# Kernel optimization log

Hardware: AMD Instinct MI355X
Metric: run time of the kernel (lower is better)

The kernel has to match this reference:

```python
import jax, jax.numpy as jnp
import numpy as np

N, HID, MAXD, B, NCLS, GRUH = 50000, 128, 16, 50, 10, 32


def setup_inputs() -> dict:
    key = jax.random.key(0)
    ks = jax.random.split(key, 18)
    s = 0.05
    nrm = lambda k, shp: (jax.random.normal(k, shp, jnp.float32) * s)
    return {
        "feature": jax.random.normal(ks[0], (N, HID), jnp.float32),
        "nbr_idx": jax.random.randint(ks[1], (N, MAXD), 0, N, dtype=jnp.int32),
        "deg": jax.random.randint(ks[2], (N,), 1, MAXD + 1, dtype=jnp.int32),
        "graph_ids": (jnp.arange(N, dtype=jnp.int32) * B) // N,
        # SAGEConv(lstm) params: LSTM(in=HID, hidden=HID) + fc_self/fc_neigh
        "lstm_Wih": nrm(ks[3], (4 * HID, HID)),
        "lstm_Whh": nrm(ks[4], (4 * HID, HID)),
        "lstm_bih": nrm(ks[5], (4 * HID,)),
        "lstm_bhh": nrm(ks[6], (4 * HID,)),
        "W_self": nrm(ks[7], (HID, HID)),
        "W_neigh": nrm(ks[8], (HID, HID)),
        "b_sage": nrm(ks[9], (HID,)),
        # GraphConv params
        "W_gc": nrm(ks[10], (HID, HID)),
        "b_gc": nrm(ks[11], (HID,)),
        # GRU params (h0=0 so weight_hh contributes nothing; only its bias matters)
        "Wih_gru": nrm(ks[12], (3 * GRUH, HID)),
        "bih_gru": nrm(ks[13], (3 * GRUH,)),
        "bhh_gru": nrm(ks[14], (3 * GRUH,)),
        # classifier (dropout is identity at eval)
        "W_cls": nrm(ks[15], (GRUH, NCLS)),
        "b_cls": nrm(ks[16], (NCLS,)),
    }


def _lstm_aggregate(feats, nbr_idx, deg, Wih, Whh, bih, bhh):
    # DGL SAGEConv 'lstm' reducer: run LSTM over each node's neighbor features,
    # take final hidden state. Implemented as a masked scan over padded lists.
    n, hdim = feats.shape
    h0 = jnp.zeros((n, hdim), feats.dtype)

    def step(carry, t):
        h, c = carry
        x = feats[jnp.take(nbr_idx, t, axis=1)]  # [N, HID] gather of t-th neighbor
        gates = x @ Wih.T + bih + h @ Whh.T + bhh
        i, f, g, o = jnp.split(gates, 4, axis=-1)  # torch gate order i,f,g,o
        c_new = jax.nn.sigmoid(f) * c + jax.nn.sigmoid(i) * jnp.tanh(g)
        h_new = jax.nn.sigmoid(o) * jnp.tanh(c_new)
        valid = (t < deg)[:, None]
        return (jnp.where(valid, h_new, h), jnp.where(valid, c_new, c)), None

    (hT, _), _ = jax.lax.scan(step, (h0, h0), jnp.arange(nbr_idx.shape[1]))
    return hT  # hidden at each node's last valid neighbor


def _graph_conv(h, nbr_idx, deg, W, b):
    # DGL GraphConv norm='both': D^-1/2 A D^-1/2 h W + b
    n, maxd = nbr_idx.shape
    norm = jax.lax.rsqrt(jnp.maximum(deg.astype(h.dtype), 1.0))
    hn = h * norm[:, None]
    mask = (jnp.arange(maxd, dtype=jnp.int32)[None, :] < deg[:, None]).astype(h.dtype)
    contrib = hn[nbr_idx.reshape(-1)] * mask.reshape(-1)[:, None]  # [N*MAXD, HID]
    dst = jnp.repeat(jnp.arange(n, dtype=jnp.int32), maxd)
    agg = jax.ops.segment_sum(contrib, dst, num_segments=n)
    return (agg * norm[:, None]) @ W + b


def _gru_step(x, Wih, bih, bhh):
    # single GRU step with h0 = 0 (seq_len == 1 in the original view(1, N, H))
    gh = x @ Wih.T + bih  # [N, 3*GRUH]
    xr, xz, xn = jnp.split(gh, 3, axis=-1)  # torch gate order r,z,n
    br, bz, bn = jnp.split(bhh, 3)
    r = jax.nn.sigmoid(xr + br)
    z = jax.nn.sigmoid(xz + bz)
    nst = jnp.tanh(xn + r * bn)
    return (1.0 - z) * nst  # h' = (1-z)*n + z*h0, h0 = 0


def reference(feature, nbr_idx, deg, graph_ids, lstm_Wih, lstm_Whh, lstm_bih,
              lstm_bhh, W_self, W_neigh, b_sage, W_gc, b_gc, Wih_gru, bih_gru,
              bhh_gru, W_cls, b_cls):
    # conv4: SAGEConv lstm -> relu
    h_nei = _lstm_aggregate(feature, nbr_idx, deg, lstm_Wih, lstm_Whh, lstm_bih, lstm_bhh)
    h = jax.nn.relu(feature @ W_self + h_nei @ W_neigh + b_sage)
    # conv2: GraphConv -> relu
    h = jax.nn.relu(_graph_conv(h, nbr_idx, deg, W_gc, b_gc))
    # GRU over seq_len=1, batch=N
    out = _gru_step(h, Wih_gru, bih_gru, bhh_gru)  # [N, 32]
    # dgl.mean_nodes: per-graph mean pool
    sums = jax.ops.segment_sum(out, graph_ids, num_segments=B)
    cnts = jax.ops.segment_sum(jnp.ones((out.shape[0],), out.dtype), graph_ids, num_segments=B)
    hg = sums / cnts[:, None]
    # classify (Dropout is identity in eval)
    return hg @ W_cls + b_cls  # [B, NCLS]
```

## Files before the change

### kernel.cpp

```cpp
#include <hip/hip_runtime.h>
#include <hip/hip_bf16.h>


#define NN     50000
#define HIDD   128
#define MAXD   16
#define NGRAPH 50
#define NCLSS  10
#define GRUH   32

typedef __attribute__((ext_vector_type(8))) short s16x8;
typedef __attribute__((ext_vector_type(4))) float f32x4;
typedef __hip_bfloat16 bf16;

#define MFMA16(a,b,c)  __builtin_amdgcn_mfma_f32_16x16x32_bf16((a),(b),(c),0,0,0)

__device__ __forceinline__ float bf2f(bf16 x) { return __bfloat162float(x); }
__device__ __forceinline__ bf16  f2bf(float x) { return __float2bfloat16(x); }
__device__ __forceinline__ s16x8 ldfrag(const bf16* p) { return *(const s16x8*)p; }

__device__ __forceinline__ s16x8 ldfrag_f32(const float* p) {
  const float4 a = *(const float4*)p;
  const float4 b = *(const float4*)(p + 4);
  union { s16x8 v; bf16 h[8]; } r;
  r.h[0] = f2bf(a.x); r.h[1] = f2bf(a.y); r.h[2] = f2bf(a.z); r.h[3] = f2bf(a.w);
  r.h[4] = f2bf(b.x); r.h[5] = f2bf(b.y); r.h[6] = f2bf(b.z); r.h[7] = f2bf(b.w);
  return r.v;
}

__device__ __forceinline__ float sigf(float x) {
  return __builtin_amdgcn_rcpf(1.0f + __expf(-x));
}
__device__ __forceinline__ float tanhf_(float x) {
  return 1.0f - 2.0f * __builtin_amdgcn_rcpf(1.0f + __expf(2.0f * x));
}

__device__ __forceinline__ unsigned packbf2(float a, float b) {
  union { bf16 h; unsigned short u; } x, y;
  x.h = f2bf(a); y.h = f2bf(b);
  return (unsigned)x.u | ((unsigned)y.u << 16);
}
__device__ __forceinline__ float lo2f(unsigned u) { return __uint_as_float(u << 16); }
__device__ __forceinline__ float hi2f(unsigned u) { return __uint_as_float(u & 0xffff0000u); }

__device__ __forceinline__ void lgkm_barrier() {
  asm volatile("s_waitcnt lgkmcnt(0)\n\ts_barrier" ::: "memory");
}

__global__ __launch_bounds__(256) void prep_kernel(const float* __restrict__ Wih,
                            const float* __restrict__ Whh, const float* __restrict__ bih,
                            const float* __restrict__ bhh, const float* __restrict__ Wself,
                            const float* __restrict__ Wneigh, const float* __restrict__ Wgc,
                            const float* __restrict__ Wgru,
                            bf16* WihB, bf16* WhhB, bf16* WsT, bf16* WnT,
                            bf16* WgT, bf16* WgruB, float* biasS,
                            int* hist, float* psums) {
  if (blockIdx.x == 0) {
    for (int i = threadIdx.x; i < 34; i += 256) hist[i] = 0;
    for (int i = threadIdx.x; i < NGRAPH * GRUH + NGRAPH; i += 256) psums[i] = 0.f;
  }
  const int total = 2 * 65536 + 3 * 16384 + 12288 + 512;
  int stride = gridDim.x * blockDim.x;
  for (int idx = blockIdx.x * blockDim.x + threadIdx.x; idx < total; idx += stride) {
    int j = idx;
    if (j < 65536) { WihB[j] = f2bf(Wih[j]); continue; }
    j -= 65536;
    if (j < 65536) { WhhB[j] = f2bf(Whh[j]); continue; }
    j -= 65536;
    if (j < 16384) { int c = j >> 7, k = j & 127; WsT[j] = f2bf(Wself[k * HIDD + c]); continue; }
    j -= 16384;
    if (j < 16384) { int c = j >> 7, k = j & 127; WnT[j] = f2bf(Wneigh[k * HIDD + c]); continue; }
    j -= 16384;
    if (j < 16384) { int c = j >> 7, k = j & 127; WgT[j] = f2bf(Wgc[k * HIDD + c]); continue; }
    j -= 16384;
    if (j < 12288) { WgruB[j] = f2bf(Wgru[j]); continue; }
    j -= 12288;
    biasS[j] = bih[j] + bhh[j];
  }
}

__global__ __launch_bounds__(256) void hist_kernel(const int* __restrict__ deg, int* hist) {
  __shared__ int lh[17];
  const int tid = threadIdx.x;
  if (tid < 17) lh[tid] = 0;
  __syncthreads();
  const int i = blockIdx.x * 256 + tid;
  if (i < NN) atomicAdd(&lh[deg[i]], 1);
  __syncthreads();
  if (tid < 17 && lh[tid]) atomicAdd(&hist[tid], lh[tid]);
}

__global__ __launch_bounds__(256) void scatter_kernel(const int* __restrict__ deg,
                                                      const int* __restrict__ hist,
                                                      int* __restrict__ resv,
                                                      int* __restrict__ perm) {
  __shared__ int lh[17], lbase[17], lpos[17];
  const int tid = threadIdx.x;
  if (tid < 17) { lh[tid] = 0; lpos[tid] = 0; }
  __syncthreads();
  const int i = blockIdx.x * 256 + tid;
  const int d = (i < NN) ? deg[i] : -1;
  if (d >= 0) atomicAdd(&lh[d], 1);
  __syncthreads();
  if (tid < 17) {
    int pre = 0;
    for (int k = tid + 1; k < 17; ++k) pre += hist[k];
    lbase[tid] = pre + (lh[tid] ? atomicAdd(&resv[tid], lh[tid]) : 0);
  }
  __syncthreads();
  if (d >= 0) {
    const int p = lbase[d] + atomicAdd(&lpos[d], 1);
    perm[p] = i;
  }
}

__global__ __launch_bounds__(256) void ggemm_kernel(const float* __restrict__ featF,
                                                    const bf16* __restrict__ WihB,
                                                    const float* __restrict__ biasS,
                                                    bf16* __restrict__ Gp) {
  __shared__ __align__(16) bf16 Gs[32][520];
  const int lane = threadIdx.x & 63, wave = threadIdx.x >> 6;
  const int l15 = lane & 15, quad = lane >> 4;
  const int nb = blockIdx.x * 64;
  const int tid = threadIdx.x;

  s16x8 Bx[4][4];
#pragma unroll
  for (int nt = 0; nt < 4; ++nt) {
    int arow = nb + nt * 16 + l15; if (arow >= NN) arow = NN - 1;
#pragma unroll
    for (int kt = 0; kt < 4; ++kt)
      Bx[nt][kt] = ldfrag_f32(featF + (size_t)arow * HIDD + kt * 32 + quad * 8);
  }

#pragma unroll
  for (int pass = 0; pass < 2; ++pass) {
    for (int hg = wave * 8; hg < wave * 8 + 8; ++hg) {
      const int wr = (l15 & 3) * HIDD + hg * 4 + (l15 >> 2);
      s16x8 Aw[4];
#pragma unroll
      for (int kt = 0; kt < 4; ++kt)
        Aw[kt] = ldfrag(WihB + (size_t)wr * HIDD + kt * 32 + quad * 8);
      const int hcol = hg * 4 + quad;
      const int gbase = (hcol >> 3) * 32 + (hcol & 3) * 8 + ((hcol >> 2) & 1) * 4;
      float b0 = biasS[0 * HIDD + hcol], b1 = biasS[1 * HIDD + hcol];
      float b2 = biasS[2 * HIDD + hcol], b3 = biasS[3 * HIDD + hcol];
#pragma unroll
      for (int nt2 = 0; nt2 < 2; ++nt2) {
        const int nt = pass * 2 + nt2;
        f32x4 acc = {0.f, 0.f, 0.f, 0.f};
#pragma unroll
        for (int kt = 0; kt < 4; ++kt)
          acc = MFMA16(Aw[kt], Bx[nt][kt], acc);
        unsigned u0 = packbf2(acc[0] + b0, acc[1] + b1);
        unsigned u1 = packbf2(acc[2] + b2, acc[3] + b3);
        *(uint2*)(&Gs[nt2 * 16 + l15][gbase]) = make_uint2(u0, u1);
      }
    }
    __syncthreads();
    for (int e = tid; e < 2048; e += 256) {
      const int r = e >> 6, off = (e & 63) * 8;
      const int node = nb + pass * 32 + r;
      if (node < NN)
        *(s16x8*)(Gp + (size_t)node * 512 + off) = *(const s16x8*)(&Gs[r][off]);
    }
    __syncthreads();
  }
}

__global__ __launch_bounds__(1024, 4) void lstm_kernel(const bf16* __restrict__ Gp,
                                                       const bf16* __restrict__ WhhB,
                                                       const float* __restrict__ featF,
                                                       const bf16* __restrict__ WsT,
                                                       const bf16* __restrict__ WnT,
                                                       const float* __restrict__ b_sage,
                                                       const int* __restrict__ nbr_idx,
                                                       const int* __restrict__ deg,
                                                       const int* __restrict__ perm,
                                                       bf16* __restrict__ h1n) {
  __shared__ __align__(16) bf16 Hs[2][64 * 128];
  __shared__ int nbr_s[16 * 64];
  __shared__ int nodes_s[64];
  __shared__ int degs_s[64];

  const int tid = threadIdx.x;
  const int lane = tid & 63, w = tid >> 6;
  const int l15 = lane & 15, quad = lane >> 4;
  const int base = blockIdx.x * 64;

  if (tid < 64) {
    const int gi = base + tid;
    const int nd = (gi < NN) ? perm[gi] : -1;
    nodes_s[tid] = nd;
    degs_s[tid] = (nd >= 0) ? deg[nd] : 0;
  }
  __syncthreads();
  {
    const int row = tid & 63, t = tid >> 6;
    const int nd = nodes_s[row];
    nbr_s[t * 64 + row] = (nd >= 0) ? nbr_idx[nd * MAXD + t] : 0;
  }

  s16x8 Bh[2][4];
#pragma unroll
  for (int gt = 0; gt < 2; ++gt) {
    const int wr = (l15 & 3) * HIDD + w * 8 + gt * 4 + (l15 >> 2);
#pragma unroll
    for (int kt = 0; kt < 4; ++kt) {
      Bh[gt][kt] = ldfrag(WhhB + (size_t)wr * HIDD + kt * 32 + quad * 8);
      asm volatile("" : "+v"(Bh[gt][kt]));
    }
  }

  __syncthreads();
  const int maxdeg = degs_s[0];

  int mydeg[4];
#pragma unroll
  for (int nt = 0; nt < 4; ++nt) mydeg[nt] = degs_s[nt * 16 + l15];

  const int gofs = w * 32 + quad * 8;

  float cst[2][4] = {{0.f, 0.f, 0.f, 0.f}, {0.f, 0.f, 0.f, 0.f}};
  float hprev[2][4] = {{0.f, 0.f, 0.f, 0.f}, {0.f, 0.f, 0.f, 0.f}};

  for (int t = 0; t < maxdeg; ++t) {
    const int cur = t & 1, nxt = cur ^ 1;

    uint2 gx[2][4];
#pragma unroll
    for (int nt = 0; nt < 4; ++nt) {
      const int nb1 = nbr_s[t * 64 + nt * 16 + l15];
      const uint4 g4 = *(const uint4*)(Gp + (size_t)nb1 * 512 + gofs);
      gx[0][nt] = make_uint2(g4.x, g4.y);
      gx[1][nt] = make_uint2(g4.z, g4.w);
    }

    f32x4 acc[2][4];
#pragma unroll
    for (int gt = 0; gt < 2; ++gt)
#pragma unroll
      for (int nt = 0; nt < 4; ++nt) acc[gt][nt] = (f32x4){0.f, 0.f, 0.f, 0.f};

    if (t > 0) {
      __builtin_amdgcn_s_setprio(1);
#pragma unroll
      for (int kt = 0; kt < 4; ++kt) {
#pragma unroll
        for (int nt = 0; nt < 4; ++nt) {
          const int row = nt * 16 + l15;
          const s16x8 ah = ldfrag(Hs[cur] + row * 128 + (((kt * 4 + quad) ^ l15) * 8));
#pragma unroll
          for (int gt = 0; gt < 2; ++gt)
            acc[gt][nt] = MFMA16(Bh[gt][kt], ah, acc[gt][nt]);
        }
      }
      __builtin_amdgcn_s_setprio(0);
    }

#pragma unroll
    for (int gt = 0; gt < 2; ++gt) {
      const int col = w * 8 + gt * 4 + quad;
#pragma unroll
      for (int nt = 0; nt < 4; ++nt) {
        const int row = nt * 16 + l15;
        const uint2 g = gx[gt][nt];
        const float g_i = acc[gt][nt][0] + lo2f(g.x);
        const float g_f = acc[gt][nt][1] + hi2f(g.x);
        const float g_g = acc[gt][nt][2] + lo2f(g.y);
        const float g_o = acc[gt][nt][3] + hi2f(g.y);
        const float iv = sigf(g_i), fv = sigf(g_f);
        const float gv = tanhf_(g_g), ov = sigf(g_o);
        const float cn = fv * cst[gt][nt] + iv * gv;
        const float hn_new = ov * tanhf_(cn);
        const bool act = (t < mydeg[nt]);
        if (act) cst[gt][nt] = cn;
        const float hn = act ? hn_new : hprev[gt][nt];
        hprev[gt][nt] = hn;
        Hs[nxt][row * 128 + ((w ^ (row & 15)) * 8) + (col & 7)] = f2bf(hn);
      }
    }
    lgkm_barrier();
  }

  const bf16* Hf = Hs[maxdeg & 1];
  {
    const int rq = w & 3, cp = w >> 2;
    const int rowA = rq * 16 + l15;
    const int ndA = nodes_s[rowA];
    const int ndA2 = (ndA >= 0) ? ndA : 0;
    s16x8 Fa[4], Ha[4];
#pragma unroll
    for (int kt = 0; kt < 4; ++kt) {
      Fa[kt] = ldfrag_f32(featF + (size_t)ndA2 * HIDD + kt * 32 + quad * 8);
      Ha[kt] = ldfrag(Hf + rowA * 128 + (((kt * 4 + quad) ^ l15) * 8));
    }
    int ndC[4]; float nrmC[4];
#pragma unroll
    for (int r = 0; r < 4; ++r) {
      const int rowC = rq * 16 + quad * 4 + r;
      ndC[r] = nodes_s[rowC];
      const int dd = degs_s[rowC];
      nrmC[r] = rsqrtf((float)((dd > 0) ? dd : 1));
    }
#pragma unroll
    for (int cc = 0; cc < 2; ++cc) {
      const int col = (cp * 2 + cc) * 16 + l15;
      f32x4 acc = {0.f, 0.f, 0.f, 0.f};
#pragma unroll
      for (int kt = 0; kt < 4; ++kt) {
        acc = MFMA16(Fa[kt], ldfrag(WsT + col * HIDD + kt * 32 + quad * 8), acc);
        acc = MFMA16(Ha[kt], ldfrag(WnT + col * HIDD + kt * 32 + quad * 8), acc);
      }
      const float bb = b_sage[col];
#pragma unroll
      for (int r = 0; r < 4; ++r)
        if (ndC[r] >= 0)
          h1n[(size_t)ndC[r] * HIDD + col] = f2bf(fmaxf(acc[r] + bb, 0.f) * nrmC[r]);
    }
  }
}

__global__ __launch_bounds__(256) void aggru_kernel(const bf16* __restrict__ h1n,
                                                    const int* __restrict__ nbr_idx,
                                                    const int* __restrict__ deg,
                                                    const int* __restrict__ gids,
                                                    const bf16* __restrict__ WgT,
                                                    const float* __restrict__ b_gc,
                                                    const bf16* __restrict__ WgruB,
                                                    const float* __restrict__ bih,
                                                    const float* __restrict__ bhh,
                                                    float* __restrict__ psums,
                                                    float* __restrict__ pcnts) {
  __shared__ __align__(16) bf16 Ag[64 * 136];
  __shared__ __align__(16) bf16 H2[64 * 136];
  __shared__ int nbrL[64 * 16];
  __shared__ float psl[2 * GRUH];
  __shared__ float pcl[2];
  const int tid = threadIdx.x;
  const int lane = tid & 63, wave = tid >> 6;
  const int l15 = lane & 15, quad = lane >> 4;
  const int nbb = blockIdx.x * 64;
  const int nb = nbb + wave * 16;

  if (tid < 2 * GRUH) psl[tid] = 0.f;
  if (tid < 2) pcl[tid] = 0.f;

  for (int e = tid; e < 64 * 16; e += 256) {
    const int node = nbb + (e >> 4);
    nbrL[e] = (node < NN) ? nbr_idx[node * MAXD + (e & 15)] : 0;
  }
  __syncthreads();

  {
    const int myn = tid >> 2;
    const int node = nbb + myn;
    const int seg = (tid & 3) * 32;
    const int d = (node < NN) ? deg[node] : 0;
    float accv[32];
#pragma unroll
    for (int k = 0; k < 32; ++k) accv[k] = 0.f;
#pragma unroll 2
    for (int j = 0; j < d; ++j) {
      const int nbr = nbrL[myn * 16 + j];
      const bf16* rp = h1n + (size_t)nbr * HIDD + seg;
#pragma unroll
      for (int f = 0; f < 4; ++f) {
        union { s16x8 v; unsigned u[4]; } t_;
        t_.v = ldfrag(rp + f * 8);
#pragma unroll
        for (int p = 0; p < 4; ++p) {
          accv[f * 8 + 2 * p]     += lo2f(t_.u[p]);
          accv[f * 8 + 2 * p + 1] += hi2f(t_.u[p]);
        }
      }
    }
    const float nm = (d > 0) ? rsqrtf((float)d) : 0.f;
#pragma unroll
    for (int f = 0; f < 4; ++f) {
      union { s16x8 v; bf16 h[8]; } o;
#pragma unroll
      for (int k = 0; k < 8; ++k) o.h[k] = f2bf(accv[f * 8 + k] * nm);
      *(s16x8*)(Ag + myn * 136 + seg + f * 8) = o.v;
    }
  }
  __syncthreads();

  s16x8 A[4];
#pragma unroll
  for (int kt = 0; kt < 4; ++kt)
    A[kt] = ldfrag(Ag + (wave * 16 + l15) * 136 + kt * 32 + quad * 8);
  for (int ct = 0; ct < 8; ++ct) {
    const int col = ct * 16 + l15;
    f32x4 acc = {0.f, 0.f, 0.f, 0.f};
#pragma unroll
    for (int kt = 0; kt < 4; ++kt)
      acc = MFMA16(A[kt], ldfrag(WgT + col * HIDD + kt * 32 + quad * 8), acc);
    const float bb = b_gc[col];
#pragma unroll
    for (int r = 0; r < 4; ++r)
      H2[(wave * 16 + quad * 4 + r) * 136 + col] = f2bf(fmaxf(acc[r] + bb, 0.f));
  }
  __syncthreads();

  s16x8 A2[4];
#pragma unroll
  for (int kt = 0; kt < 4; ++kt)
    A2[kt] = ldfrag(H2 + (wave * 16 + l15) * 136 + kt * 32 + quad * 8);
  f32x4 acc[6];
#pragma unroll
  for (int ct = 0; ct < 6; ++ct) {
    f32x4 a = {0.f, 0.f, 0.f, 0.f};
#pragma unroll
    for (int kt = 0; kt < 4; ++kt)
      a = MFMA16(A2[kt], ldfrag(WgruB + (ct * 16 + l15) * HIDD + kt * 32 + quad * 8), a);
    acc[ct] = a;
  }

  const int g0 = gids[nbb];
  int mynode[4], mygs[4];
#pragma unroll
  for (int r = 0; r < 4; ++r) {
    const int nd = nb + quad * 4 + r;
    mynode[r] = nd;
    mygs[r] = (nd < NN) ? (gids[nd] - g0) : 0;
  }
#pragma unroll
  for (int u = 0; u < 2; ++u) {
    const int cu = 16 * u + l15;
    const float br = bih[cu] + bhh[cu];
    const float bz = bih[32 + cu] + bhh[32 + cu];
    const float bni = bih[64 + cu];
    const float bnh = bhh[64 + cu];
#pragma unroll
    for (int r = 0; r < 4; ++r) {
      if (mynode[r] < NN) {
        const float rv = sigf(acc[u][r] + br);
        const float zv = sigf(acc[2 + u][r] + bz);
        const float nv = tanhf_(acc[4 + u][r] + bni + rv * bnh);
        const float v = (1.f - zv) * nv;
        atomicAdd(&psl[mygs[r] * GRUH + cu], v);
        if (u == 0 && l15 == 0) atomicAdd(&pcl[mygs[r]], 1.f);
      }
    }
  }
  __syncthreads();
  if (tid < 2 * GRUH) {
    const int s = tid >> 5, c = tid & 31;
    const float vv = psl[tid];
    if (vv != 0.f && g0 + s < NGRAPH) atomicAdd(&psums[(g0 + s) * GRUH + c], vv);
  }
  if (tid < 2) {
    if (pcl[tid] != 0.f && g0 + tid < NGRAPH) atomicAdd(&pcnts[g0 + tid], pcl[tid]);
  }
}

__global__ __launch_bounds__(256) void pool_final_kernel(const float* __restrict__ sums,
                                                         const float* __restrict__ cnts,
                                                         const float* __restrict__ Wcls,
                                                         const float* __restrict__ bcls,
                                                         float* __restrict__ out) {
  const int idx = blockIdx.x * blockDim.x + threadIdx.x;
  if (idx >= NGRAPH * NCLSS) return;
  const int g = idx / NCLSS, k = idx % NCLSS;
  const float inv = 1.0f / cnts[g];
  float acc = bcls[k];
#pragma unroll
  for (int cc = 0; cc < GRUH; ++cc)
    acc += sums[g * GRUH + cc] * inv * Wcls[cc * NCLSS + k];
  out[idx] = acc;
}

extern "C" void kernel_launch(void* const* d_in, const int* in_sizes, int n_in,
                              void* d_out, int out_size, void* d_ws, size_t ws_size,
                              hipStream_t stream) {
  const float* feature  = (const float*)d_in[0];
  const int*   nbr_idx  = (const int*)d_in[1];
  const int*   deg      = (const int*)d_in[2];
  const int*   gids     = (const int*)d_in[3];
  const float* lstm_Wih = (const float*)d_in[4];
  const float* lstm_Whh = (const float*)d_in[5];
  const float* lstm_bih = (const float*)d_in[6];
  const float* lstm_bhh = (const float*)d_in[7];
  const float* W_self   = (const float*)d_in[8];
  const float* W_neigh  = (const float*)d_in[9];
  const float* b_sage   = (const float*)d_in[10];
  const float* W_gc     = (const float*)d_in[11];
  const float* b_gc     = (const float*)d_in[12];
  const float* Wih_gru  = (const float*)d_in[13];
  const float* bih_gru  = (const float*)d_in[14];
  const float* bhh_gru  = (const float*)d_in[15];
  const float* W_cls    = (const float*)d_in[16];
  const float* b_cls    = (const float*)d_in[17];

  char* ws = (char*)d_ws;
  bf16*  h1nB  = (bf16*)(ws + 0);
  bf16*  Gp    = (bf16*)(ws + 12800000);
  const size_t wo = 64000000;
  bf16*  WihB  = (bf16*)(ws + wo);
  bf16*  WhhB  = (bf16*)(ws + wo + 131072);
  bf16*  WsT   = (bf16*)(ws + wo + 262144);
  bf16*  WnT   = (bf16*)(ws + wo + 294912);
  bf16*  WgT   = (bf16*)(ws + wo + 327680);
  bf16*  WgruB = (bf16*)(ws + wo + 360448);
  float* biasS = (float*)(ws + wo + 385024);
  int*   perm  = (int*)(ws + 64500000);
  int*   hist  = (int*)(ws + 64800000);
  int*   resv  = hist + 17;
  float* psums = (float*)(ws + 64801216);
  float* pcnts = psums + NGRAPH * GRUH;

  prep_kernel<<<754, 256, 0, stream>>>(lstm_Wih, lstm_Whh, lstm_bih, lstm_bhh,
                                       W_self, W_neigh, W_gc, Wih_gru,
                                       WihB, WhhB, WsT, WnT, WgT, WgruB, biasS,
                                       hist, psums);
  hist_kernel<<<196, 256, 0, stream>>>(deg, hist);
  scatter_kernel<<<196, 256, 0, stream>>>(deg, hist, resv, perm);
  ggemm_kernel<<<782, 256, 0, stream>>>(feature, WihB, biasS, Gp);
  lstm_kernel<<<782, 1024, 0, stream>>>(Gp, WhhB, feature, WsT, WnT, b_sage,
                                        nbr_idx, deg, perm, h1nB);
  aggru_kernel<<<782, 256, 0, stream>>>(h1nB, nbr_idx, deg, gids, WgT, b_gc,
                                        WgruB, bih_gru, bhh_gru, psums, pcnts);
  pool_final_kernel<<<2, 256, 0, stream>>>(psums, pcnts, W_cls, b_cls, (float*)d_out);
}
```

Baseline: 378.9 us.

## Fuse histogram, scatter, and final pooling into neighboring kernels to cut launches

Per-block degree histograms are now computed inside the weight-prep kernel and written to per-block slots. The scatter/permutation blocks are appended to the input-gate GEMM launch, so the two no longer need separate kernels. The final classifier runs in the last block of the aggregation kernel through an atomic ticket. This drops seven launches to four, at the cost of every scatter block re-summing 196 partial histograms and the usual last-block fence pattern.

```diff
diff --git a/kernel.cpp b/kernel.cpp
--- a/kernel.cpp
+++ b/kernel.cpp
@@ -51,13 +51,25 @@
                             const float* __restrict__ Whh, const float* __restrict__ bih,
                             const float* __restrict__ bhh, const float* __restrict__ Wself,
                             const float* __restrict__ Wneigh, const float* __restrict__ Wgc,
-                            const float* __restrict__ Wgru,
+                            const float* __restrict__ Wgru, const int* __restrict__ deg,
                             bf16* WihB, bf16* WhhB, bf16* WsT, bf16* WnT,
                             bf16* WgT, bf16* WgruB, float* biasS,
-                            int* hist, float* psums) {
+                            int* histp, int* resv, float* psums, int* done) {
+  __shared__ int lh[17];
+  const int tid = threadIdx.x;
+  const bool histblk = (blockIdx.x < 196);
+  if (histblk) {
+    if (tid < 17) lh[tid] = 0;
+    __syncthreads();
+    const int i = blockIdx.x * 256 + tid;
+    if (i < NN) atomicAdd(&lh[deg[i]], 1);
+    __syncthreads();
+    if (tid < 17) histp[blockIdx.x * 17 + tid] = lh[tid];
+  }
   if (blockIdx.x == 0) {
-    for (int i = threadIdx.x; i < 34; i += 256) hist[i] = 0;
-    for (int i = threadIdx.x; i < NGRAPH * GRUH + NGRAPH; i += 256) psums[i] = 0.f;
+    for (int i = tid; i < 17; i += 256) resv[i] = 0;
+    for (int i = tid; i < NGRAPH * GRUH + NGRAPH; i += 256) psums[i] = 0.f;
+    if (tid == 0) *done = 0;
   }
   const int total = 2 * 65536 + 3 * 16384 + 12288 + 512;
   int stride = gridDim.x * blockDim.x;
@@ -79,50 +91,46 @@
   }
 }
 
-__global__ __launch_bounds__(256) void hist_kernel(const int* __restrict__ deg, int* hist) {
-  __shared__ int lh[17];
+__global__ __launch_bounds__(256) void sg_kernel(const float* __restrict__ featF,
+                                                 const bf16* __restrict__ WihB,
+                                                 const float* __restrict__ biasS,
+                                                 bf16* __restrict__ Gp,
+                                                 const int* __restrict__ deg,
+                                                 const int* __restrict__ histp,
+                                                 int* __restrict__ resv,
+                                                 int* __restrict__ perm) {
   const int tid = threadIdx.x;
-  if (tid < 17) lh[tid] = 0;
-  __syncthreads();
-  const int i = blockIdx.x * 256 + tid;
-  if (i < NN) atomicAdd(&lh[deg[i]], 1);
-  __syncthreads();
-  if (tid < 17 && lh[tid]) atomicAdd(&hist[tid], lh[tid]);
-}
-
-__global__ __launch_bounds__(256) void scatter_kernel(const int* __restrict__ deg,
-                                                      const int* __restrict__ hist,
-                                                      int* __restrict__ resv,
-                                                      int* __restrict__ perm) {
-  __shared__ int lh[17], lbase[17], lpos[17];
-  const int tid = threadIdx.x;
-  if (tid < 17) { lh[tid] = 0; lpos[tid] = 0; }
-  __syncthreads();
-  const int i = blockIdx.x * 256 + tid;
-  const int d = (i < NN) ? deg[i] : -1;
-  if (d >= 0) atomicAdd(&lh[d], 1);
-  __syncthreads();
-  if (tid < 17) {
-    int pre = 0;
-    for (int k = tid + 1; k < 17; ++k) pre += hist[k];
-    lbase[tid] = pre + (lh[tid] ? atomicAdd(&resv[tid], lh[tid]) : 0);
-  }
-  __syncthreads();
-  if (d >= 0) {
-    const int p = lbase[d] + atomicAdd(&lpos[d], 1);
-    perm[p] = i;
-  }
-}
-
-__global__ __launch_bounds__(256) void ggemm_kernel(const float* __restrict__ featF,
-                                                    const bf16* __restrict__ WihB,
-                                                    const float* __restrict__ biasS,
-                                                    bf16* __restrict__ Gp) {
+  if (blockIdx.x >= 782) {
+    __shared__ int lh[17], lbase[17], lpos[17], gh[17];
+    const int sb = blockIdx.x - 782;
+    if (tid < 17) { lh[tid] = 0; lpos[tid] = 0; }
+    __syncthreads();
+    const int i = sb * 256 + tid;
+    const int d = (i < NN) ? deg[i] : -1;
+    if (d >= 0) atomicAdd(&lh[d], 1);
+    __syncthreads();
+    if (tid < 17) {
+      int s = 0;
+      for (int b = 0; b < 196; ++b) s += histp[b * 17 + tid];
+      gh[tid] = s;
+    }
+    __syncthreads();
+    if (tid < 17) {
+      int pre = 0;
+      for (int k = tid + 1; k < 17; ++k) pre += gh[k];
+      lbase[tid] = pre + (lh[tid] ? atomicAdd(&resv[tid], lh[tid]) : 0);
+    }
+    __syncthreads();
+    if (d >= 0) {
+      const int p = lbase[d] + atomicAdd(&lpos[d], 1);
+      perm[p] = i;
+    }
+    return;
+  }
   __shared__ __align__(16) bf16 Gs[32][520];
-  const int lane = threadIdx.x & 63, wave = threadIdx.x >> 6;
+  const int lane = tid & 63, wave = tid >> 6;
   const int l15 = lane & 15, quad = lane >> 4;
   const int nb = blockIdx.x * 64;
-  const int tid = threadIdx.x;
 
   s16x8 Bx[4][4];
 #pragma unroll
@@ -331,12 +339,17 @@
                                                     const float* __restrict__ bih,
                                                     const float* __restrict__ bhh,
                                                     float* __restrict__ psums,
-                                                    float* __restrict__ pcnts) {
+                                                    float* __restrict__ pcnts,
+                                                    int* __restrict__ done,
+                                                    const float* __restrict__ Wcls,
+                                                    const float* __restrict__ bcls,
+                                                    float* __restrict__ out) {
   __shared__ __align__(16) bf16 Ag[64 * 136];
   __shared__ __align__(16) bf16 H2[64 * 136];
   __shared__ int nbrL[64 * 16];
   __shared__ float psl[2 * GRUH];
   __shared__ float pcl[2];
+  __shared__ int ticket_s;
   const int tid = threadIdx.x;
   const int lane = tid & 63, wave = tid >> 6;
   const int l15 = lane & 15, quad = lane >> 4;
@@ -453,22 +466,26 @@
   if (tid < 2) {
     if (pcl[tid] != 0.f && g0 + tid < NGRAPH) atomicAdd(&pcnts[g0 + tid], pcl[tid]);
   }
-}
-
-__global__ __launch_bounds__(256) void pool_final_kernel(const float* __restrict__ sums,
-                                                         const float* __restrict__ cnts,
-                                                         const float* __restrict__ Wcls,
-                                                         const float* __restrict__ bcls,
-                                                         float* __restrict__ out) {
-  const int idx = blockIdx.x * blockDim.x + threadIdx.x;
-  if (idx >= NGRAPH * NCLSS) return;
-  const int g = idx / NCLSS, k = idx % NCLSS;
-  const float inv = 1.0f / cnts[g];
-  float acc = bcls[k];
-#pragma unroll
-  for (int cc = 0; cc < GRUH; ++cc)
-    acc += sums[g * GRUH + cc] * inv * Wcls[cc * NCLSS + k];
-  out[idx] = acc;
+
+  __threadfence();
+  if (tid == 0) ticket_s = atomicAdd(done, 1);
+  __syncthreads();
+  if (ticket_s == (int)gridDim.x - 1) {
+    __shared__ float ps[NGRAPH * GRUH];
+    __shared__ float pc[NGRAPH];
+    for (int i = tid; i < NGRAPH * GRUH; i += 256) ps[i] = atomicAdd(&psums[i], 0.f);
+    for (int i = tid; i < NGRAPH; i += 256) pc[i] = atomicAdd(&pcnts[i], 0.f);
+    __syncthreads();
+    for (int idx = tid; idx < NGRAPH * NCLSS; idx += 256) {
+      const int g = idx / NCLSS, k = idx % NCLSS;
+      const float inv = 1.0f / pc[g];
+      float accо = bcls[k];
+#pragma unroll
+      for (int cc = 0; cc < GRUH; ++cc)
+        accо += ps[g * GRUH + cc] * inv * Wcls[cc * NCLSS + k];
+      out[idx] = accо;
+    }
+  }
 }
 
 extern "C" void kernel_launch(void* const* d_in, const int* in_sizes, int n_in,
@@ -505,21 +522,20 @@
   bf16*  WgruB = (bf16*)(ws + wo + 360448);
   float* biasS = (float*)(ws + wo + 385024);
   int*   perm  = (int*)(ws + 64500000);
-  int*   hist  = (int*)(ws + 64800000);
-  int*   resv  = hist + 17;
-  float* psums = (float*)(ws + 64801216);
-  float* pcnts = psums + NGRAPH * GRUH;
+  int*   histp = (int*)(ws + 64800000);
+  int*   resv  = (int*)(ws + 64814000);
+  float* psums = (float*)(ws + 64815000);
+  float* pcnts = (float*)(ws + 64821400);
+  int*   done  = (int*)(ws + 64821600);
 
   prep_kernel<<<754, 256, 0, stream>>>(lstm_Wih, lstm_Whh, lstm_bih, lstm_bhh,
-                                       W_self, W_neigh, W_gc, Wih_gru,
+                                       W_self, W_neigh, W_gc, Wih_gru, deg,
                                        WihB, WhhB, WsT, WnT, WgT, WgruB, biasS,
-                                       hist, psums);
-  hist_kernel<<<196, 256, 0, stream>>>(deg, hist);
-  scatter_kernel<<<196, 256, 0, stream>>>(deg, hist, resv, perm);
-  ggemm_kernel<<<782, 256, 0, stream>>>(feature, WihB, biasS, Gp);
+                                       histp, resv, psums, done);
+  sg_kernel<<<978, 256, 0, stream>>>(feature, WihB, biasS, Gp, deg, histp, resv, perm);
   lstm_kernel<<<782, 1024, 0, stream>>>(Gp, WhhB, feature, WsT, WnT, b_sage,
                                         nbr_idx, deg, perm, h1nB);
   aggru_kernel<<<782, 256, 0, stream>>>(h1nB, nbr_idx, deg, gids, WgT, b_gc,
-                                        WgruB, bih_gru, bhh_gru, psums, pcnts);
-  pool_final_kernel<<<2, 256, 0, stream>>>(psums, pcnts, W_cls, b_cls, (float*)d_out);
-}
+                                        WgruB, bih_gru, bhh_gru, psums, pcnts,
+                                        done, W_cls, b_cls, (float*)d_out);
+}
```

Measured after the change: 407.8 us. +7.6%, slower.
